# Kernel optimization log

Measured on AMD Instinct MI355X. Metric: run time of the kernel, lower is better.

Reference implementation:

```python
import jax, jax.numpy as jnp
import numpy as np

B, L, DIN, DM, NL = 2, 1024, 512, 1024, 4
E, N, R, K = 2048, 16, 64, 4  # d_inner, d_state, dt_rank, d_conv


def setup_inputs() -> dict:
    key = jax.random.key(0)
    ks = iter(jax.random.split(key, 32))
    rn = lambda sh, s=1.0: jax.random.normal(next(ks), sh, jnp.float32) * s
    A_init = jnp.broadcast_to(jnp.arange(1, N + 1, dtype=jnp.float32), (NL, E, N))
    return dict(
        x=rn((B, L, DIN)),
        z=rn((B, L, DIN)),
        ip_w=rn((DM, DIN), 0.02), ip_b=jnp.zeros((DM,), jnp.float32),
        ln_w=jnp.ones((NL, DM), jnp.float32), ln_b=jnp.zeros((NL, DM), jnp.float32),
        inproj_w=rn((NL, 2 * E, DM), 0.02),
        conv_w=rn((NL, E, K), 0.1), conv_b=jnp.zeros((NL, E), jnp.float32),
        xproj_w=rn((NL, R + 2 * N, E), 0.02),
        dtproj_w=rn((NL, E, R), 0.05), dtproj_b=rn((NL, E), 0.1),
        A_log=jnp.log(A_init),
        Dp=jnp.ones((NL, E), jnp.float32),
        outproj_w=rn((NL, DM, E), 0.02),
        fnorm_w=jnp.ones((DM,), jnp.float32), fnorm_b=jnp.zeros((DM,), jnp.float32),
        op_w=rn((DIN, DM), 0.02), op_b=jnp.zeros((DIN,), jnp.float32),
    )


def layernorm(x, w, b, eps=1e-5):
    m = x.mean(-1, keepdims=True)
    v = ((x - m) ** 2).mean(-1, keepdims=True)
    return (x - m) * jax.lax.rsqrt(v + eps) * w + b


def dwconv_causal(xm, w, b):
    # xm: (B, L, E); w: (E, K) depthwise kernel; causal left padding
    xc = xm.transpose(0, 2, 1)  # (B, E, L)
    out = jax.lax.conv_general_dilated(
        xc, w[:, None, :], (1,), [(K - 1, 0)],
        feature_group_count=E, dimension_numbers=('NCH', 'OIH', 'NCH'))
    return (out + b[:, None]).transpose(0, 2, 1)


def selective_scan(u, dt, A, Bm, Cm, D):
    # u, dt: (B, L, E); A: (E, N); Bm, Cm: (B, L, N); D: (E,)
    h0 = jnp.zeros((u.shape[0], E, N), u.dtype)

    def step(h, inp):
        dt_t, u_t, B_t, C_t = inp  # (B,E),(B,E),(B,N),(B,N)
        dA = jnp.exp(dt_t[..., None] * A)                      # (B, E, N)
        h = dA * h + (dt_t * u_t)[..., None] * B_t[:, None, :]  # (B, E, N)
        y = jnp.einsum('ben,bn->be', h, C_t)
        return h, y

    _, ys = jax.lax.scan(step, h0, (dt.transpose(1, 0, 2), u.transpose(1, 0, 2),
                                    Bm.transpose(1, 0, 2), Cm.transpose(1, 0, 2)))
    return ys.transpose(1, 0, 2) + u * D  # (B, L, E)


def mamba_block(x, inproj_w, conv_w, conv_b, xproj_w, dtproj_w, dtproj_b, A_log, Dp, outproj_w):
    xz = jnp.einsum('bld,ed->ble', x, inproj_w)  # (B, L, 2E)
    xm, zg = xz[..., :E], xz[..., E:]
    xm = jax.nn.silu(dwconv_causal(xm, conv_w, conv_b))
    x_dbl = jnp.einsum('ble,re->blr', xm, xproj_w)  # (B, L, R+2N)
    dt = jax.nn.softplus(jnp.einsum('blr,er->ble', x_dbl[..., :R], dtproj_w) + dtproj_b)
    Bm = x_dbl[..., R:R + N]
    Cm = x_dbl[..., R + N:]
    A = -jnp.exp(A_log)  # (E, N)
    y = selective_scan(xm, dt, A, Bm, Cm, Dp)
    y = y * jax.nn.silu(zg)
    return jnp.einsum('ble,de->bld', y, outproj_w)


def reference(x, z, ip_w, ip_b, ln_w, ln_b, inproj_w, conv_w, conv_b, xproj_w,
              dtproj_w, dtproj_b, A_log, Dp, outproj_w, fnorm_w, fnorm_b, op_w, op_b):
    # z is accepted but unused, matching the original forward(x, z)
    h = jnp.einsum('bld,hd->blh', x, ip_w) + ip_b
    for l in range(NL):
        hn = layernorm(h, ln_w[l], ln_b[l])
        h = h + mamba_block(hn, inproj_w[l], conv_w[l], conv_b[l], xproj_w[l],
                            dtproj_w[l], dtproj_b[l], A_log[l], Dp[l], outproj_w[l])
    h = layernorm(h, fnorm_w, fnorm_b)
    return jnp.einsum('blh,oh->blo', h, op_w) + op_b
```

## Files before the change

### kernel.cpp

```cpp
#include <hip/hip_runtime.h>
#include <math.h>

#define BB 2
#define LL 1024
#define DIN_ 512
#define DM_ 1024
#define NL_ 4
#define EE 2048
#define NN 16
#define RR 64
#define KK 4

#define NC 32
#define CT 32

typedef unsigned short ushort_t;
typedef unsigned int uint_t;

using frag_ab = __attribute__((ext_vector_type(8))) short;
using frag_cd = __attribute__((ext_vector_type(4))) float;

__device__ __forceinline__ float softplus_f(float x) {
    return fmaxf(x, 0.f) + log1pf(expf(-fabsf(x)));
}
__device__ __forceinline__ float silu_fast(float x) {
    return x / (1.f + __expf(-x));
}
__device__ __forceinline__ float bf2f(ushort_t x) {
    return __uint_as_float((uint_t)x << 16);
}
__device__ __forceinline__ ushort_t f2bf(float x) {
    uint_t u = __float_as_uint(x);
    uint_t r = (u + 0x7fffu + ((u >> 16) & 1u)) >> 16;
    return (ushort_t)r;
}
__device__ __forceinline__ void gload_lds16(const void* g, void* l) {
    __builtin_amdgcn_global_load_lds(
        (const __attribute__((address_space(1))) void*)g,
        (__attribute__((address_space(3))) void*)l, 16, 0, 0);
}

__global__ __launch_bounds__(256) void cvt_bf16_kernel(
    ushort_t* __restrict__ o, const float* __restrict__ in, int n4)
{
    int i = blockIdx.x * 256 + threadIdx.x;
    if (i >= n4) return;
    float4 v = ((const float4*)in)[i];
    ushort4 u;
    u.x = f2bf(v.x); u.y = f2bf(v.y); u.z = f2bf(v.z); u.w = f2bf(v.w);
    ((ushort4*)o)[i] = u;
}

__global__ __launch_bounds__(256) void zero_kernel(float* __restrict__ p, int n4)
{
    int i = blockIdx.x * 256 + threadIdx.x;
    if (i < n4) ((float4*)p)[i] = make_float4(0.f, 0.f, 0.f, 0.f);
}

__global__ __launch_bounds__(256) void rowbias_kernel(
    float* __restrict__ dst, const float* __restrict__ bias, int n4, int total4)
{
    int i = blockIdx.x * 256 + threadIdx.x;
    if (i >= total4) return;
    int c = i % n4;
    ((float4*)dst)[i] = ((const float4*)bias)[c];
}

template <int EPI, int NT, int OUTBF>
__global__ __launch_bounds__(256) void mgemm_kernel(
    void* __restrict__ Cp, const ushort_t* __restrict__ A,
    const ushort_t* __restrict__ W, const float* __restrict__ bias,
    int N, int K, int lda, int ldw, int ldc)
{
    __shared__ __attribute__((aligned(16))) ushort_t As[2][8 * 512];
    __shared__ __attribute__((aligned(16))) ushort_t Bs[2][NT * 512];

    const int tid = threadIdx.x;
    const int w = tid >> 6;
    const int lane = tid & 63;
    const int r = lane & 15;
    const int q = lane >> 4;
    const int m0 = blockIdx.y * 128;
    const int n0 = blockIdx.x * (NT * 16);
    const int wm = w >> 1;
    const int wn = w & 1;
    const int NWT = NT / 2;

    frag_cd acc[4][NWT];
#pragma unroll
    for (int i = 0; i < 4; i++)
#pragma unroll
        for (int j = 0; j < NWT; j++)
#pragma unroll
            for (int t = 0; t < 4; t++) acc[i][j][t] = 0.f;

    size_t koff = (EPI == 4) ? (size_t)blockIdx.z * K : 0;
    const ushort_t* Ab = A + (size_t)m0 * lda + koff;
    const ushort_t* Wb = W + (size_t)n0 * ldw + koff;

    const int NFRAG = 8 + NT;
    auto stage = [&](int k0, int buf) {
        for (int F = w; F < NFRAG; F += 4) {
            if (F < 8) {
                gload_lds16(Ab + (size_t)(F * 16 + r) * lda + k0 + q * 8,
                            &As[buf][F * 512]);
            } else {
                int nt = F - 8;
                if (n0 + nt * 16 + r < N)
                    gload_lds16(Wb + (size_t)(nt * 16 + r) * ldw + k0 + q * 8,
                                &Bs[buf][nt * 512]);
            }
        }
    };

    stage(0, 0);
    int buf = 0;
    for (int k0 = 0; k0 < K; k0 += 32) {
        __syncthreads();
        if (k0 + 32 < K) stage(k0 + 32, buf ^ 1);
        frag_ab af[4], bf[NWT];
#pragma unroll
        for (int i = 0; i < 4; i++)
            af[i] = *(const frag_ab*)(&As[buf][(wm * 4 + i) * 512] + lane * 8);
#pragma unroll
        for (int j = 0; j < NWT; j++)
            bf[j] = *(const frag_ab*)(&Bs[buf][(wn * NWT + j) * 512] + lane * 8);
#pragma unroll
        for (int i = 0; i < 4; i++)
#pragma unroll
            for (int j = 0; j < NWT; j++)
                acc[i][j] = __builtin_amdgcn_mfma_f32_16x16x32_bf16(
                    af[i], bf[j], acc[i][j], 0, 0, 0);
        buf ^= 1;
    }

    float* Cf = (float*)Cp;
    ushort_t* Cb = (ushort_t*)Cp;
#pragma unroll
    for (int i = 0; i < 4; i++) {
        int mrow = m0 + (wm * 4 + i) * 16 + q * 4;
#pragma unroll
        for (int j = 0; j < NWT; j++) {
            int col = n0 + (wn * NWT + j) * 16 + r;
            if (col >= N) continue;
            float bv = (EPI == 1 || EPI == 2) ? bias[col] : 0.f;
#pragma unroll
            for (int t = 0; t < 4; t++) {
                float v = acc[i][j][t];
                size_t idx = (size_t)(mrow + t) * ldc + col;
                if (EPI == 4) { atomicAdd(Cf + idx, v); continue; }
                if (EPI == 1) v += bv;
                if (EPI == 2) v = softplus_f(v + bv);
                if (EPI == 3) v += Cf[idx];
                if (OUTBF) Cb[idx] = f2bf(v);
                else       Cf[idx] = v;
            }
        }
    }
}

__global__ __launch_bounds__(256) void layernorm_kernel(
    ushort_t* __restrict__ out, const float* __restrict__ in,
    const float* __restrict__ w, const float* __restrict__ b)
{
    const int row = blockIdx.x;
    const int tid = threadIdx.x;
    float4 v = ((const float4*)(in + (size_t)row * DM_))[tid];
    float s = v.x + v.y + v.z + v.w;
    float sq = v.x * v.x + v.y * v.y + v.z * v.z + v.w * v.w;
#pragma unroll
    for (int off = 32; off; off >>= 1) {
        s += __shfl_down(s, off);
        sq += __shfl_down(sq, off);
    }
    __shared__ float ls[4], lq[4];
    int wid = tid >> 6;
    if ((tid & 63) == 0) { ls[wid] = s; lq[wid] = sq; }
    __syncthreads();
    float S = ls[0] + ls[1] + ls[2] + ls[3];
    float Q = lq[0] + lq[1] + lq[2] + lq[3];
    float mean = S * (1.f / DM_);
    float var = Q * (1.f / DM_) - mean * mean;
    float inv = rsqrtf(var + 1e-5f);
    float4 wv = ((const float4*)w)[tid];
    float4 bv = ((const float4*)b)[tid];
    ushort4 o;
    o.x = f2bf((v.x - mean) * inv * wv.x + bv.x);
    o.y = f2bf((v.y - mean) * inv * wv.y + bv.y);
    o.z = f2bf((v.z - mean) * inv * wv.z + bv.z);
    o.w = f2bf((v.w - mean) * inv * wv.w + bv.w);
    ((ushort4*)(out + (size_t)row * DM_))[tid] = o;
}

__global__ __launch_bounds__(256) void conv_silu_kernel(
    ushort_t* __restrict__ xm, const ushort_t* __restrict__ xz,
    const float* __restrict__ cw, const float* __restrict__ cb)
{
    const int e = blockIdx.x * 256 + threadIdx.x;
    const int t0 = blockIdx.y * 4;
    const int b = blockIdx.z;
    const ushort_t* X = xz + (size_t)b * LL * 2 * EE + e;
    float4 w4 = ((const float4*)cw)[e];
    float wk[4] = {w4.x, w4.y, w4.z, w4.w};
    float cbv = cb[e];
    float v[7];
#pragma unroll
    for (int k = 0; k < 7; k++) {
        int t = t0 - 3 + k;
        v[k] = (t >= 0) ? bf2f(X[(size_t)t * 2 * EE]) : 0.f;
    }
    ushort_t* Y = xm + ((size_t)b * LL + t0) * EE + e;
#pragma unroll
    for (int j = 0; j < 4; j++) {
        float acc = cbv;
#pragma unroll
        for (int k = 0; k < 4; k++) acc = fmaf(wk[k], v[j + k], acc);
        Y[(size_t)j * EE] = f2bf(silu_fast(acc));
    }
}

__global__ __launch_bounds__(256) void scan_phase1_kernel(
    float* __restrict__ Pg, float* __restrict__ Sg,
    const float* __restrict__ dt, const ushort_t* __restrict__ u,
    const float* __restrict__ xdb, const float* __restrict__ A_log)
{
    const int tid = threadIdx.x;
    const int e = blockIdx.x * 256 + tid;
    const int c = blockIdx.y;
    const int b = blockIdx.z;
    const int t0 = c * CT;

    __shared__ float Bs[CT][16];
    {
        int tt = tid >> 3;
        int jj = tid & 7;
        if (jj < 4) {
            float4 v = *(const float4*)(xdb + ((size_t)(b * LL + t0 + tt) * 96 + 64 + jj * 4));
            *(float4*)&Bs[tt][jj * 4] = v;
        }
    }
    __syncthreads();

    float Ae[16];
#pragma unroll
    for (int k = 0; k < 4; k++) {
        float4 a = *(const float4*)(A_log + (size_t)e * NN + k * 4);
        Ae[k * 4 + 0] = -__expf(a.x);
        Ae[k * 4 + 1] = -__expf(a.y);
        Ae[k * 4 + 2] = -__expf(a.z);
        Ae[k * 4 + 3] = -__expf(a.w);
    }

    float S[16];
#pragma unroll
    for (int n = 0; n < 16; n++) S[n] = 0.f;
    float Dsum = 0.f;

    const float* dt_p = dt + (size_t)(b * LL + t0) * EE + e;
    const ushort_t* u_p = u + (size_t)(b * LL + t0) * EE + e;

    float dtv = dt_p[0];
    float uv = bf2f(u_p[0]);
#pragma unroll 4
    for (int i = 0; i < CT; i++) {
        int ip = (i + 1 < CT) ? i + 1 : i;
        float dtn = dt_p[(size_t)ip * EE];
        float un = bf2f(u_p[(size_t)ip * EE]);
        float dtu = dtv * uv;
        Dsum += dtv;
        float Bv[16];
#pragma unroll
        for (int k = 0; k < 4; k++)
            *(float4*)&Bv[k * 4] = *(const float4*)&Bs[i][k * 4];
#pragma unroll
        for (int n = 0; n < 16; n++) {
            float da = __expf(dtv * Ae[n]);
            S[n] = fmaf(da, S[n], dtu * Bv[n]);
        }
        dtv = dtn; uv = un;
    }

    size_t o = ((size_t)(b * NC + c) * EE + e) * 16;
#pragma unroll
    for (int k = 0; k < 4; k++) {
        float4 p4;
        p4.x = __expf(Dsum * Ae[k * 4 + 0]);
        p4.y = __expf(Dsum * Ae[k * 4 + 1]);
        p4.z = __expf(Dsum * Ae[k * 4 + 2]);
        p4.w = __expf(Dsum * Ae[k * 4 + 3]);
        *(float4*)(Pg + o + k * 4) = p4;
        *(float4*)(Sg + o + k * 4) = *(float4*)&S[k * 4];
    }
}

__global__ __launch_bounds__(256) void scan_combine_kernel(
    float* __restrict__ Pg, const float* __restrict__ Sg)
{
    const int f = blockIdx.x * 256 + threadIdx.x;
    const int b = blockIdx.y;
    float h = 0.f;
    for (int c = 0; c < NC; c++) {
        size_t o = (size_t)(b * NC + c) * EE * 16 + f;
        float p = Pg[o];
        float s = Sg[o];
        h = fmaf(p, h, s);
        Pg[o] = h;
    }
}

__global__ __launch_bounds__(256) void scan_phase2_kernel(
    ushort_t* __restrict__ y, const float* __restrict__ Pg,
    const float* __restrict__ dt, const ushort_t* __restrict__ u,
    const float* __restrict__ xdb, const ushort_t* __restrict__ xz,
    const float* __restrict__ A_log, const float* __restrict__ Dp)
{
    const int tid = threadIdx.x;
    const int e = blockIdx.x * 256 + tid;
    const int c = blockIdx.y;
    const int b = blockIdx.z;
    const int t0 = c * CT;

    __shared__ float Bs[CT][16], Cs[CT][16];
    {
        int tt = tid >> 3;
        int jj = tid & 7;
        float4 v = *(const float4*)(xdb + ((size_t)(b * LL + t0 + tt) * 96 + 64 + jj * 4));
        if (jj < 4) *(float4*)&Bs[tt][jj * 4] = v;
        else        *(float4*)&Cs[tt][(jj - 4) * 4] = v;
    }
    __syncthreads();

    float Ae[16];
#pragma unroll
    for (int k = 0; k < 4; k++) {
        float4 a = *(const float4*)(A_log + (size_t)e * NN + k * 4);
        Ae[k * 4 + 0] = -__expf(a.x);
        Ae[k * 4 + 1] = -__expf(a.y);
        Ae[k * 4 + 2] = -__expf(a.z);
        Ae[k * 4 + 3] = -__expf(a.w);
    }

    float h[16];
    if (c == 0) {
#pragma unroll
        for (int n = 0; n < 16; n++) h[n] = 0.f;
    } else {
        size_t o = ((size_t)(b * NC + (c - 1)) * EE + e) * 16;
#pragma unroll
        for (int k = 0; k < 4; k++)
            *(float4*)&h[k * 4] = *(const float4*)(Pg + o + k * 4);
    }

    const float Dv = Dp[e];
    const float* dt_p = dt + (size_t)(b * LL + t0) * EE + e;
    const ushort_t* u_p = u + (size_t)(b * LL + t0) * EE + e;
    const ushort_t* zg_p = xz + (size_t)(b * LL + t0) * 2 * EE + EE + e;
    ushort_t* y_p = y + (size_t)(b * LL + t0) * EE + e;

    float dtv = dt_p[0];
    float uv = bf2f(u_p[0]);
    float zv = bf2f(zg_p[0]);
#pragma unroll 4
    for (int i = 0; i < CT; i++) {
        int ip = (i + 1 < CT) ? i + 1 : i;
        float dtn = dt_p[(size_t)ip * EE];
        float un = bf2f(u_p[(size_t)ip * EE]);
        float zn = bf2f(zg_p[(size_t)ip * 2 * EE]);
        float dtu = dtv * uv;
        float Bv[16], Cv[16];
#pragma unroll
        for (int k = 0; k < 4; k++) {
            *(float4*)&Bv[k * 4] = *(const float4*)&Bs[i][k * 4];
            *(float4*)&Cv[k * 4] = *(const float4*)&Cs[i][k * 4];
        }
        float yv = 0.f;
#pragma unroll
        for (int n = 0; n < 16; n++) {
            float da = __expf(dtv * Ae[n]);
            h[n] = fmaf(da, h[n], dtu * Bv[n]);
            yv = fmaf(h[n], Cv[n], yv);
        }
        y_p[(size_t)i * EE] = f2bf((yv + uv * Dv) * silu_fast(zv));
        dtv = dtn; uv = un; zv = zn;
    }
}

extern "C" void kernel_launch(void* const* d_in, const int* in_sizes, int n_in,
                              void* d_out, int out_size, void* d_ws, size_t ws_size,
                              hipStream_t stream)
{
    const float* x = (const float*)d_in[0];
    const float* ip_w = (const float*)d_in[2];
    const float* ip_b = (const float*)d_in[3];
    const float* ln_w = (const float*)d_in[4];
    const float* ln_b = (const float*)d_in[5];
    const float* inproj_w = (const float*)d_in[6];
    const float* conv_w = (const float*)d_in[7];
    const float* conv_b = (const float*)d_in[8];
    const float* xproj_w = (const float*)d_in[9];
    const float* dtproj_w = (const float*)d_in[10];
    const float* dtproj_b = (const float*)d_in[11];
    const float* A_log = (const float*)d_in[12];
    const float* Dp = (const float*)d_in[13];
    const float* outproj_w = (const float*)d_in[14];
    const float* fnorm_w = (const float*)d_in[15];
    const float* fnorm_b = (const float*)d_in[16];
    const float* op_w = (const float*)d_in[17];
    const float* op_b = (const float*)d_in[18];
    float* out = (float*)d_out;

    const size_t BL = (size_t)BB * LL;

    float* fp = (float*)d_ws;
    float* h = fp;           fp += BL * DM_;
    float* xdb = fp;         fp += BL * 96;
    float* dtb = fp;         fp += BL * EE;
    float* Pg = fp;          fp += (size_t)BB * NC * EE * 16;
    float* Sg = fp;          fp += (size_t)BB * NC * EE * 16;
    ushort_t* us = (ushort_t*)fp;
    ushort_t* xb = us;       us += BL * DIN_;
    ushort_t* hnb = us;      us += BL * DM_;
    ushort_t* xzb = us;      us += BL * 2 * EE;
    ushort_t* xm = us;       us += BL * EE;
    ushort_t* xdbb = us;     us += BL * 96;
    ushort_t* yb = us;       us += BL * EE;
    ushort_t* ipwb = us;     us += (size_t)DM_ * DIN_;
    ushort_t* inprojb = us;  us += (size_t)NL_ * 2 * EE * DM_;
    ushort_t* xprojb = us;   us += (size_t)NL_ * 96 * EE;
    ushort_t* dtprojb = us;  us += (size_t)NL_ * EE * RR;
    ushort_t* outprojb = us; us += (size_t)NL_ * DM_ * EE;
    ushort_t* opwb = us;     us += (size_t)DIN_ * DM_;

    dim3 blk(256);
    auto cvt = [&](ushort_t* dst, const float* src, size_t n) {
        int n4 = (int)(n / 4);
        cvt_bf16_kernel<<<dim3((n4 + 255) / 256), blk, 0, stream>>>(dst, src, n4);
    };

    cvt(xb, x, BL * DIN_);
    cvt(ipwb, ip_w, (size_t)DM_ * DIN_);
    cvt(inprojb, inproj_w, (size_t)NL_ * 2 * EE * DM_);
    cvt(xprojb, xproj_w, (size_t)NL_ * 96 * EE);
    cvt(dtprojb, dtproj_w, (size_t)NL_ * EE * RR);
    cvt(outprojb, outproj_w, (size_t)NL_ * DM_ * EE);
    cvt(opwb, op_w, (size_t)DIN_ * DM_);

    rowbias_kernel<<<dim3((int)(BL * DM_ / 4 + 255) / 256), blk, 0, stream>>>(
        h, ip_b, DM_ / 4, (int)(BL * DM_ / 4));
    mgemm_kernel<4, 4, 0><<<dim3(DM_ / 64, BL / 128, 2), blk, 0, stream>>>(
        h, xb, ipwb, nullptr, DM_, DIN_ / 2, DIN_, DIN_, DM_);

    for (int l = 0; l < NL_; l++) {
        layernorm_kernel<<<dim3(BL), blk, 0, stream>>>(hnb, h, ln_w + l * DM_, ln_b + l * DM_);
        mgemm_kernel<0, 8, 1><<<dim3(2 * EE / 128, BL / 128), blk, 0, stream>>>(
            xzb, hnb, inprojb + (size_t)l * 2 * EE * DM_, nullptr,
            2 * EE, DM_, DM_, DM_, 2 * EE);
        conv_silu_kernel<<<dim3(EE / 256, LL / 4, BB), blk, 0, stream>>>(
            xm, xzb, conv_w + l * EE * KK, conv_b + l * EE);
        zero_kernel<<<dim3((int)(BL * 96 / 4 + 255) / 256), blk, 0, stream>>>(xdb, (int)(BL * 96 / 4));
        mgemm_kernel<4, 8, 0><<<dim3(1, BL / 128, 16), blk, 0, stream>>>(
            xdb, xm, xprojb + (size_t)l * 96 * EE, nullptr,
            96, EE / 16, EE, EE, 96);
        cvt(xdbb, xdb, BL * 96);
        mgemm_kernel<2, 8, 0><<<dim3(EE / 128, BL / 128), blk, 0, stream>>>(
            dtb, xdbb, dtprojb + (size_t)l * EE * RR, dtproj_b + l * EE,
            EE, RR, 96, RR, EE);

        scan_phase1_kernel<<<dim3(EE / 256, NC, BB), blk, 0, stream>>>(
            Pg, Sg, dtb, xm, xdb, A_log + (size_t)l * EE * NN);
        scan_combine_kernel<<<dim3(EE * 16 / 256, BB), blk, 0, stream>>>(Pg, Sg);
        scan_phase2_kernel<<<dim3(EE / 256, NC, BB), blk, 0, stream>>>(
            yb, Pg, dtb, xm, xdb, xzb, A_log + (size_t)l * EE * NN, Dp + l * EE);

        mgemm_kernel<4, 8, 0><<<dim3(DM_ / 128, BL / 128, 4), blk, 0, stream>>>(
            h, yb, outprojb + (size_t)l * DM_ * EE, nullptr,
            DM_, EE / 4, EE, EE, DM_);
    }

    layernorm_kernel<<<dim3(BL), blk, 0, stream>>>(hnb, h, fnorm_w, fnorm_b);
    rowbias_kernel<<<dim3((int)(BL * DIN_ / 4 + 255) / 256), blk, 0, stream>>>(
        out, op_b, DIN_ / 4, (int)(BL * DIN_ / 4));
    mgemm_kernel<4, 4, 0><<<dim3(DIN_ / 64, BL / 128, 4), blk, 0, stream>>>(
        out, hnb, opwb, nullptr, DIN_, DM_ / 4, DM_, DM_, DIN_);
}
```

Before: 1.010 ms.

## Replace split-K atomics with partial buffers and fused reduce-layernorm kernels

```diff
diff --git a/kernel.cpp b/kernel.cpp
--- a/kernel.cpp
+++ b/kernel.cpp
@@ -51,26 +51,11 @@
     ((ushort4*)o)[i] = u;
 }
 
-__global__ __launch_bounds__(256) void zero_kernel(float* __restrict__ p, int n4)
-{
-    int i = blockIdx.x * 256 + threadIdx.x;
-    if (i < n4) ((float4*)p)[i] = make_float4(0.f, 0.f, 0.f, 0.f);
-}
-
-__global__ __launch_bounds__(256) void rowbias_kernel(
-    float* __restrict__ dst, const float* __restrict__ bias, int n4, int total4)
-{
-    int i = blockIdx.x * 256 + threadIdx.x;
-    if (i >= total4) return;
-    int c = i % n4;
-    ((float4*)dst)[i] = ((const float4*)bias)[c];
-}
-
 template <int EPI, int NT, int OUTBF>
 __global__ __launch_bounds__(256) void mgemm_kernel(
     void* __restrict__ Cp, const ushort_t* __restrict__ A,
     const ushort_t* __restrict__ W, const float* __restrict__ bias,
-    int N, int K, int lda, int ldw, int ldc)
+    int N, int K, int lda, int ldw, int ldc, int pstride)
 {
     __shared__ __attribute__((aligned(16))) ushort_t As[2][8 * 512];
     __shared__ __attribute__((aligned(16))) ushort_t Bs[2][NT * 512];
@@ -94,7 +79,7 @@
 #pragma unroll
             for (int t = 0; t < 4; t++) acc[i][j][t] = 0.f;
 
-    size_t koff = (EPI == 4) ? (size_t)blockIdx.z * K : 0;
+    size_t koff = (EPI == 5) ? (size_t)blockIdx.z * K : 0;
     const ushort_t* Ab = A + (size_t)m0 * lda + koff;
     const ushort_t* Wb = W + (size_t)n0 * ldw + koff;
 
@@ -136,6 +121,7 @@
 
     float* Cf = (float*)Cp;
     ushort_t* Cb = (ushort_t*)Cp;
+    float* Cpart = (EPI == 5) ? Cf + (size_t)blockIdx.z * pstride : Cf;
 #pragma unroll
     for (int i = 0; i < 4; i++) {
         int mrow = m0 + (wm * 4 + i) * 16 + q * 4;
@@ -143,15 +129,13 @@
         for (int j = 0; j < NWT; j++) {
             int col = n0 + (wn * NWT + j) * 16 + r;
             if (col >= N) continue;
-            float bv = (EPI == 1 || EPI == 2) ? bias[col] : 0.f;
+            float bv = (EPI == 2) ? bias[col] : 0.f;
 #pragma unroll
             for (int t = 0; t < 4; t++) {
                 float v = acc[i][j][t];
                 size_t idx = (size_t)(mrow + t) * ldc + col;
-                if (EPI == 4) { atomicAdd(Cf + idx, v); continue; }
-                if (EPI == 1) v += bv;
+                if (EPI == 5) { Cpart[idx] = v; continue; }
                 if (EPI == 2) v = softplus_f(v + bv);
-                if (EPI == 3) v += Cf[idx];
                 if (OUTBF) Cb[idx] = f2bf(v);
                 else       Cf[idx] = v;
             }
@@ -159,13 +143,28 @@
     }
 }
 
-__global__ __launch_bounds__(256) void layernorm_kernel(
-    ushort_t* __restrict__ out, const float* __restrict__ in,
-    const float* __restrict__ w, const float* __restrict__ b)
+__global__ __launch_bounds__(256) void reduce_ln_kernel(
+    float* __restrict__ h, ushort_t* __restrict__ hn,
+    const float* __restrict__ parts, int nparts, int pstride4,
+    const float* __restrict__ bias,
+    const float* __restrict__ w, const float* __restrict__ b, int hasres)
 {
     const int row = blockIdx.x;
     const int tid = threadIdx.x;
-    float4 v = ((const float4*)(in + (size_t)row * DM_))[tid];
+    const int i4 = row * (DM_ / 4) + tid;
+
+    float4 v = make_float4(0.f, 0.f, 0.f, 0.f);
+    if (hasres) v = ((const float4*)h)[i4];
+    for (int p = 0; p < nparts; p++) {
+        float4 t = ((const float4*)parts)[(size_t)p * pstride4 + i4];
+        v.x += t.x; v.y += t.y; v.z += t.z; v.w += t.w;
+    }
+    if (bias) {
+        float4 t = ((const float4*)bias)[tid];
+        v.x += t.x; v.y += t.y; v.z += t.z; v.w += t.w;
+    }
+    ((float4*)h)[i4] = v;
+
     float s = v.x + v.y + v.z + v.w;
     float sq = v.x * v.x + v.y * v.y + v.z * v.z + v.w * v.w;
 #pragma unroll
@@ -189,7 +188,40 @@
     o.y = f2bf((v.y - mean) * inv * wv.y + bv.y);
     o.z = f2bf((v.z - mean) * inv * wv.z + bv.z);
     o.w = f2bf((v.w - mean) * inv * wv.w + bv.w);
-    ((ushort4*)(out + (size_t)row * DM_))[tid] = o;
+    ((ushort4*)hn)[i4] = o;
+}
+
+__global__ __launch_bounds__(256) void reduce_xdb_kernel(
+    float* __restrict__ xdb, ushort_t* __restrict__ xdbb,
+    const float* __restrict__ parts, int pstride4, int total4)
+{
+    int i = blockIdx.x * 256 + threadIdx.x;
+    if (i >= total4) return;
+    float4 v = make_float4(0.f, 0.f, 0.f, 0.f);
+#pragma unroll
+    for (int p = 0; p < 16; p++) {
+        float4 t = ((const float4*)parts)[(size_t)p * pstride4 + i];
+        v.x += t.x; v.y += t.y; v.z += t.z; v.w += t.w;
+    }
+    ((float4*)xdb)[i] = v;
+    ushort4 u;
+    u.x = f2bf(v.x); u.y = f2bf(v.y); u.z = f2bf(v.z); u.w = f2bf(v.w);
+    ((ushort4*)xdbb)[i] = u;
+}
+
+__global__ __launch_bounds__(256) void reduce_bias_kernel(
+    float* __restrict__ out, const float* __restrict__ parts,
+    const float* __restrict__ bias, int pstride4, int n4, int total4)
+{
+    int i = blockIdx.x * 256 + threadIdx.x;
+    if (i >= total4) return;
+    float4 v = ((const float4*)bias)[i % n4];
+#pragma unroll
+    for (int p = 0; p < 4; p++) {
+        float4 t = ((const float4*)parts)[(size_t)p * pstride4 + i];
+        v.x += t.x; v.y += t.y; v.z += t.z; v.w += t.w;
+    }
+    ((float4*)out)[i] = v;
 }
 
 __global__ __launch_bounds__(256) void conv_silu_kernel(
@@ -417,6 +449,7 @@
     float* dtb = fp;         fp += BL * EE;
     float* Pg = fp;          fp += (size_t)BB * NC * EE * 16;
     float* Sg = fp;          fp += (size_t)BB * NC * EE * 16;
+    float* parts = dtb;
     ushort_t* us = (ushort_t*)fp;
     ushort_t* xb = us;       us += BL * DIN_;
     ushort_t* hnb = us;      us += BL * DM_;
@@ -445,26 +478,27 @@
     cvt(outprojb, outproj_w, (size_t)NL_ * DM_ * EE);
     cvt(opwb, op_w, (size_t)DIN_ * DM_);
 
-    rowbias_kernel<<<dim3((int)(BL * DM_ / 4 + 255) / 256), blk, 0, stream>>>(
-        h, ip_b, DM_ / 4, (int)(BL * DM_ / 4));
-    mgemm_kernel<4, 4, 0><<<dim3(DM_ / 64, BL / 128, 2), blk, 0, stream>>>(
-        h, xb, ipwb, nullptr, DM_, DIN_ / 2, DIN_, DIN_, DM_);
+    const int PS_DM = (int)(BL * DM_);
+
+    mgemm_kernel<5, 4, 0><<<dim3(DM_ / 64, BL / 128, 2), blk, 0, stream>>>(
+        parts, xb, ipwb, nullptr, DM_, DIN_ / 2, DIN_, DIN_, DM_, PS_DM);
+    reduce_ln_kernel<<<dim3(BL), blk, 0, stream>>>(
+        h, hnb, parts, 2, PS_DM / 4, ip_b, ln_w, ln_b, 0);
 
     for (int l = 0; l < NL_; l++) {
-        layernorm_kernel<<<dim3(BL), blk, 0, stream>>>(hnb, h, ln_w + l * DM_, ln_b + l * DM_);
         mgemm_kernel<0, 8, 1><<<dim3(2 * EE / 128, BL / 128), blk, 0, stream>>>(
             xzb, hnb, inprojb + (size_t)l * 2 * EE * DM_, nullptr,
-            2 * EE, DM_, DM_, DM_, 2 * EE);
+            2 * EE, DM_, DM_, DM_, 2 * EE, 0);
         conv_silu_kernel<<<dim3(EE / 256, LL / 4, BB), blk, 0, stream>>>(
             xm, xzb, conv_w + l * EE * KK, conv_b + l * EE);
-        zero_kernel<<<dim3((int)(BL * 96 / 4 + 255) / 256), blk, 0, stream>>>(xdb, (int)(BL * 96 / 4));
-        mgemm_kernel<4, 8, 0><<<dim3(1, BL / 128, 16), blk, 0, stream>>>(
-            xdb, xm, xprojb + (size_t)l * 96 * EE, nullptr,
-            96, EE / 16, EE, EE, 96);
-        cvt(xdbb, xdb, BL * 96);
+        mgemm_kernel<5, 8, 0><<<dim3(1, BL / 128, 16), blk, 0, stream>>>(
+            parts, xm, xprojb + (size_t)l * 96 * EE, nullptr,
+            96, EE / 16, EE, EE, 96, (int)(BL * 96));
+        reduce_xdb_kernel<<<dim3((int)(BL * 96 / 4 + 255) / 256), blk, 0, stream>>>(
+            xdb, xdbb, parts, (int)(BL * 96 / 4), (int)(BL * 96 / 4));
         mgemm_kernel<2, 8, 0><<<dim3(EE / 128, BL / 128), blk, 0, stream>>>(
             dtb, xdbb, dtprojb + (size_t)l * EE * RR, dtproj_b + l * EE,
-            EE, RR, 96, RR, EE);
+            EE, RR, 96, RR, EE, 0);
 
         scan_phase1_kernel<<<dim3(EE / 256, NC, BB), blk, 0, stream>>>(
             Pg, Sg, dtb, xm, xdb, A_log + (size_t)l * EE * NN);
@@ -472,14 +506,17 @@
         scan_phase2_kernel<<<dim3(EE / 256, NC, BB), blk, 0, stream>>>(
             yb, Pg, dtb, xm, xdb, xzb, A_log + (size_t)l * EE * NN, Dp + l * EE);
 
-        mgemm_kernel<4, 8, 0><<<dim3(DM_ / 128, BL / 128, 4), blk, 0, stream>>>(
-            h, yb, outprojb + (size_t)l * DM_ * EE, nullptr,
-            DM_, EE / 4, EE, EE, DM_);
-    }
-
-    layernorm_kernel<<<dim3(BL), blk, 0, stream>>>(hnb, h, fnorm_w, fnorm_b);
-    rowbias_kernel<<<dim3((int)(BL * DIN_ / 4 + 255) / 256), blk, 0, stream>>>(
-        out, op_b, DIN_ / 4, (int)(BL * DIN_ / 4));
-    mgemm_kernel<4, 4, 0><<<dim3(DIN_ / 64, BL / 128, 4), blk, 0, stream>>>(
-        out, hnb, opwb, nullptr, DIN_, DM_ / 4, DM_, DM_, DIN_);
-}
+        mgemm_kernel<5, 8, 0><<<dim3(DM_ / 128, BL / 128, 4), blk, 0, stream>>>(
+            parts, yb, outprojb + (size_t)l * DM_ * EE, nullptr,
+            DM_, EE / 4, EE, EE, DM_, PS_DM);
+        const float* nw = (l + 1 < NL_) ? ln_w + (l + 1) * DM_ : fnorm_w;
+        const float* nb = (l + 1 < NL_) ? ln_b + (l + 1) * DM_ : fnorm_b;
+        reduce_ln_kernel<<<dim3(BL), blk, 0, stream>>>(
+            h, hnb, parts, 4, PS_DM / 4, nullptr, nw, nb, 1);
+    }
+
+    mgemm_kernel<5, 4, 0><<<dim3(DIN_ / 64, BL / 128, 4), blk, 0, stream>>>(
+        parts, hnb, opwb, nullptr, DIN_, DM_ / 4, DM_, DM_, DIN_, (int)(BL * DIN_));
+    reduce_bias_kernel<<<dim3((int)(BL * DIN_ / 4 + 255) / 256), blk, 0, stream>>>(
+        out, parts, op_b, (int)(BL * DIN_ / 4), DIN_ / 4, (int)(BL * DIN_ / 4));
+}
```

Result: faster. 917.9 us (-9.1%).
